# Kernel tuning notes

Measured on AMD Instinct MI355X. Metric: run time of the kernel, lower is better.

The kernel has to match this reference:

```python
import jax, jax.numpy as jnp
import numpy as np

EMBED = 1024
HEADS = 16
HEAD_DIM = EMBED // HEADS


def setup_inputs() -> dict:
    key = jax.random.key(0)
    k1, k2, k3, k4, k5 = jax.random.split(key, 5)
    B, S = 4, 2048
    scale = 1.0 / np.sqrt(EMBED)
    return {
        "query_features": jax.random.normal(k1, (B, S, EMBED), dtype=jnp.float32),
        "W_qkv": jax.random.normal(k2, (EMBED, 3 * EMBED), dtype=jnp.float32) * scale,
        "b_qkv": jnp.zeros((3 * EMBED,), dtype=jnp.float32),
        "W_out": jax.random.normal(k3, (EMBED, EMBED), dtype=jnp.float32) * scale,
        "b_out": jnp.zeros((EMBED,), dtype=jnp.float32),
    }


def reference(query_features, W_qkv, b_qkv, W_out, b_out):
    B, S, E = query_features.shape
    qkv = jnp.einsum("bse,ef->bsf", query_features, W_qkv) + b_qkv  # [B,S,3E]
    q, k, v = jnp.split(qkv, 3, axis=-1)
    # split heads: [B,H,S,D]
    def heads(x):
        return x.reshape(B, S, HEADS, HEAD_DIM).transpose(0, 2, 1, 3)
    q, k, v = heads(q), heads(k), heads(v)
    scale = 1.0 / np.sqrt(HEAD_DIM)
    scores = jnp.einsum("bhqd,bhkd->bhqk", q, k) * scale
    attn = jax.nn.softmax(scores, axis=-1)
    out = jnp.einsum("bhqk,bhkd->bhqd", attn, v)  # [B,H,S,D]
    out = out.transpose(0, 2, 1, 3).reshape(B, S, E)
    return jnp.einsum("bse,ef->bsf", out, W_out) + b_out
```

## Files before the change

kernel.cpp:

```cpp
#include <hip/hip_runtime.h>
#include <hip/hip_bf16.h>
#include <stdint.h>
#include <stddef.h>

using short8  = __attribute__((ext_vector_type(8))) short;
using short4v = __attribute__((ext_vector_type(4))) short;
using int4v   = __attribute__((ext_vector_type(4))) int;
using f32x4   = __attribute__((ext_vector_type(4))) float;
typedef __hip_bfloat16 bf16_t;

__device__ __forceinline__ void glds16(const void* g, const void* l) {
  __builtin_amdgcn_global_load_lds(
      (const __attribute__((address_space(1))) void*)g,
      (__attribute__((address_space(3))) void*)l, 16, 0, 0);
}
__device__ __forceinline__ short bfbits(float x) {
  bf16_t h = __float2bfloat16(x);
  return __builtin_bit_cast(short, h);
}
__device__ __forceinline__ int pk2(float lo, float hi) {
  return __builtin_amdgcn_perm(__builtin_bit_cast(unsigned, hi),
                               __builtin_bit_cast(unsigned, lo), 0x07060302u);
}

__global__ __launch_bounds__(256)
void preprocess(const void* __restrict__ Wqkv, bf16_t* __restrict__ WqkvT,
                const void* __restrict__ Wout, bf16_t* __restrict__ WoutT,
                const void* __restrict__ Xv, bf16_t* __restrict__ Xb,
                int* __restrict__ flag) {
  __shared__ int sbad;
  __shared__ float tile[32][33];
  const int tid = threadIdx.x;
  const int bid = blockIdx.x;
  if (tid == 0) sbad = 0;
  __syncthreads();
  {
    int bad = 0;
    const unsigned short* wp = (const unsigned short*)Wqkv;
#pragma unroll
    for (int j = 0; j < 4; ++j) {
      float f = __uint_as_float((unsigned)wp[tid + j * 256] << 16);
      if (!(fabsf(f) <= 1e10f)) bad = 1;
    }
    if (bad) sbad = 1;
  }
  __syncthreads();
  const int isf = sbad;
  if (bid == 0 && tid == 0) *flag = isf;

  if (bid < 4096) {
    int bx = bid & 127;
    const int by = bid >> 7;
    const int tx = tid & 31, ty = tid >> 5;
    const void* Wv;
    bf16_t* Wt;
    int C;
    if (bx < 96) {
      Wv = Wqkv; Wt = WqkvT; C = 3072;
    } else {
      bx -= 96; Wv = Wout; Wt = WoutT; C = 1024;
    }
    const int n0 = bx * 32, k0 = by * 32;
#pragma unroll
    for (int j = 0; j < 4; ++j) {
      const int k = k0 + ty + j * 8;
      tile[ty + j * 8][tx] =
          isf ? ((const float*)Wv)[(size_t)k * C + n0 + tx]
              : __bfloat162float(((const bf16_t*)Wv)[(size_t)k * C + n0 + tx]);
    }
    __syncthreads();
#pragma unroll
    for (int j = 0; j < 4; ++j) {
      const int n = n0 + ty + j * 8;
      Wt[(size_t)n * 1024 + k0 + tx] = __float2bfloat16(tile[tx][ty + j * 8]);
    }
  } else {
    const int i = ((bid - 4096) * 256 + tid) * 4;
    if (isf) {
      const float4 v = *(const float4*)((const float*)Xv + i);
      Xb[i + 0] = __float2bfloat16(v.x);
      Xb[i + 1] = __float2bfloat16(v.y);
      Xb[i + 2] = __float2bfloat16(v.z);
      Xb[i + 3] = __float2bfloat16(v.w);
    } else {
      *(uint2*)(Xb + i) = *(const uint2*)((const bf16_t*)Xv + i);
    }
  }
}

template <int MODE>
__global__ __launch_bounds__(256)
void gemm_k(const bf16_t* __restrict__ A, const bf16_t* __restrict__ Bt,
            const void* __restrict__ biasv, void* __restrict__ Cv,
            bf16_t* __restrict__ Qo, bf16_t* __restrict__ Ko,
            bf16_t* __restrict__ Vo, int M, int N, int K,
            const int* __restrict__ flag) {
  constexpr float CSC = 0.18033688011112042f;
  __shared__ __align__(16) bf16_t lA[128 * 64];
  __shared__ __align__(16) bf16_t lB[128 * 64];

  const int isf32 = *flag;
  const int tid  = threadIdx.x;
  const int w    = tid >> 6;
  const int lane = tid & 63;
  const int lrow = lane & 15;
  const int quad = lane >> 4;
  const int m0 = blockIdx.x * 128;
  const int n0 = blockIdx.y * 128;
  const int wm = (w >> 1) * 64;
  const int wn = (w & 1) * 64;

  f32x4 acc[4][4];
  for (int i = 0; i < 4; ++i)
    for (int j = 0; j < 4; ++j)
      for (int r = 0; r < 4; ++r) acc[i][j][r] = 0.f;

  for (int kt = 0; kt < K; kt += 64) {
#pragma unroll
    for (int i = 0; i < 4; ++i) {
      const int cbase = i * 256 + w * 64;
      const int c = cbase + lane;
      const int row = c >> 3;
      const int q = (c & 7) ^ (row & 7);
      glds16(A + (size_t)(m0 + row) * K + kt + q * 8,
             (const char*)lA + cbase * 16);
      glds16(Bt + (size_t)(n0 + row) * K + kt + q * 8,
             (const char*)lB + cbase * 16);
    }
    __syncthreads();
#pragma unroll
    for (int ks = 0; ks < 2; ++ks) {
      short8 af[4], bfr[4];
#pragma unroll
      for (int mi = 0; mi < 4; ++mi) {
        const int row = wm + mi * 16 + lrow;
        const int slot = (ks * 4 + quad) ^ (row & 7);
        af[mi] = *(const short8*)((const char*)lA + row * 128 + slot * 16);
      }
#pragma unroll
      for (int ni = 0; ni < 4; ++ni) {
        const int row = wn + ni * 16 + lrow;
        const int slot = (ks * 4 + quad) ^ (row & 7);
        bfr[ni] = *(const short8*)((const char*)lB + row * 128 + slot * 16);
      }
#pragma unroll
      for (int mi = 0; mi < 4; ++mi)
#pragma unroll
        for (int ni = 0; ni < 4; ++ni)
          acc[mi][ni] = __builtin_amdgcn_mfma_f32_16x16x32_bf16(
              af[mi], bfr[ni], acc[mi][ni], 0, 0, 0);
    }
    __syncthreads();
  }

  if (MODE == 1) {
    const int sec = n0 >> 10;
    const int b = m0 >> 11;
    const int s0 = (m0 & 2047) + wm + quad * 4;
#pragma unroll
    for (int mi = 0; mi < 4; ++mi) {
#pragma unroll
      for (int ni = 0; ni < 4; ++ni) {
        const int col = n0 + wn + ni * 16 + lrow;
        const float bv = isf32 ? ((const float*)biasv)[col]
                               : __bfloat162float(((const bf16_t*)biasv)[col]);
        const int h = (col >> 6) & 15, d = col & 63;
        const int s = s0 + mi * 16;
        if (sec == 2) {
          short4v hv4;
#pragma unroll
          for (int r = 0; r < 4; ++r) hv4[r] = bfbits(acc[mi][ni][r] + bv);
          *(short4v*)(Vo + ((((size_t)b * 16 + h) * 64) + d) * 2048 + s) = hv4;
        } else if (sec == 0) {
          bf16_t* dst = Qo + ((((size_t)b * 16 + h) * 2048) + s) * 64 + d;
#pragma unroll
          for (int r = 0; r < 4; ++r)
            dst[(size_t)r * 64] = __float2bfloat16((acc[mi][ni][r] + bv) * CSC);
        } else {
          bf16_t* dst = Ko + ((((size_t)b * 16 + h) * 2048) + s) * 64 + d;
#pragma unroll
          for (int r = 0; r < 4; ++r)
            dst[(size_t)r * 64] = __float2bfloat16(acc[mi][ni][r] + bv);
        }
      }
    }
  } else {
#pragma unroll
    for (int mi = 0; mi < 4; ++mi) {
#pragma unroll
      for (int ni = 0; ni < 4; ++ni) {
        const int col = n0 + wn + ni * 16 + lrow;
        const float bv = isf32 ? ((const float*)biasv)[col]
                               : __bfloat162float(((const bf16_t*)biasv)[col]);
#pragma unroll
        for (int r = 0; r < 4; ++r) {
          const int row = m0 + wm + mi * 16 + quad * 4 + r;
          const float val = acc[mi][ni][r] + bv;
          if (isf32)
            ((float*)Cv)[(size_t)row * N + col] = val;
          else
            ((bf16_t*)Cv)[(size_t)row * N + col] = __float2bfloat16(val);
        }
      }
    }
  }
}

__global__ __launch_bounds__(256, 2)
void attn_fwd(const bf16_t* __restrict__ Q, const bf16_t* __restrict__ K,
              const bf16_t* __restrict__ Vt, bf16_t* __restrict__ AO) {
  __shared__ __align__(16) bf16_t lK[2][64 * 64];
  __shared__ __align__(16) bf16_t lV[2][64 * 64];

  const int tid  = threadIdx.x;
  const int w    = tid >> 6;
  const int lane = tid & 63;
  const int lrow = lane & 15;
  const int quad = lane >> 4;
  const int id = blockIdx.x;
  const int swz = (id & 7) * 64 + (id >> 3);
  const int bh  = swz >> 3;
  const int q0  = (swz & 7) * 256;

  const bf16_t* Qb = Q + (size_t)bh * 2048 * 64;
  const bf16_t* Kb = K + (size_t)bh * 2048 * 64;
  const bf16_t* Vb = Vt + (size_t)bh * 64 * 2048;

  const int rbase = (lrow >> 2) * 8 + (lrow & 3);
  const int fkl   = 2 * (lrow >> 2) + (lrow & 1);

  short8 aq[4][2];
#pragma unroll
  for (int qt = 0; qt < 4; ++qt)
#pragma unroll
    for (int ks = 0; ks < 2; ++ks)
      aq[qt][ks] = *(const short8*)(Qb +
          (size_t)(q0 + w * 64 + qt * 16 + lrow) * 64 + ks * 32 + quad * 8);

  short8 ones;
#pragma unroll
  for (int j = 0; j < 8; ++j) ones[j] = (short)0x3F80;

  const f32x4 zf = {0.f, 0.f, 0.f, 0.f};

  f32x4 ot[4][4];
  f32x4 lsacc[4];
#pragma unroll
  for (int dt = 0; dt < 4; ++dt)
#pragma unroll
    for (int qt = 0; qt < 4; ++qt)
#pragma unroll
      for (int r = 0; r < 4; ++r) ot[dt][qt][r] = 0.f;
#pragma unroll
  for (int qt = 0; qt < 4; ++qt)
#pragma unroll
    for (int r = 0; r < 4; ++r) lsacc[qt][r] = 0.f;

  auto stage = [&](int buf, int kt) {
#pragma unroll
    for (int i = 0; i < 2; ++i) {
      const int cbase = i * 256 + w * 64;
      const int c = cbase + lane;
      const int row = c >> 3, ch = c & 7;
      const int fk = 2 * ((row >> 3) & 3) + (row & 1);
      glds16(Kb + (size_t)(kt + row) * 64 + (ch ^ fk) * 8,
             (const char*)lK[buf] + cbase * 16);
      glds16(Vb + (size_t)row * 2048 + kt + (ch ^ (row & 7)) * 8,
             (const char*)lV[buf] + cbase * 16);
    }
  };

  auto compute = [&](const bf16_t* lKb, const bf16_t* lVb) {
#pragma unroll
    for (int g = 0; g < 2; ++g) {
      short8 ak0[2], ak1[2];
#pragma unroll
      for (int T = 0; T < 2; ++T) {
        const int row = g * 32 + T * 4 + rbase;
        ak0[T] = *(const short8*)((const char*)lKb + row * 128 +
                                  ((0 * 4 + quad) ^ fkl) * 16);
        ak1[T] = *(const short8*)((const char*)lKb + row * 128 +
                                  ((1 * 4 + quad) ^ fkl) * 16);
      }
      f32x4 sc[2][4];
      __builtin_amdgcn_s_setprio(1);
#pragma unroll
      for (int T = 0; T < 2; ++T)
#pragma unroll
        for (int qt = 0; qt < 4; ++qt)
          sc[T][qt] = __builtin_amdgcn_mfma_f32_16x16x32_bf16(
              ak0[T], aq[qt][0], zf, 0, 0, 0);
#pragma unroll
      for (int T = 0; T < 2; ++T)
#pragma unroll
        for (int qt = 0; qt < 4; ++qt)
          sc[T][qt] = __builtin_amdgcn_mfma_f32_16x16x32_bf16(
              ak1[T], aq[qt][1], sc[T][qt], 0, 0, 0);
      __builtin_amdgcn_s_setprio(0);

      short8 pb[4];
#pragma unroll
      for (int qt = 0; qt < 4; ++qt) {
        float p[8];
#pragma unroll
        for (int T = 0; T < 2; ++T)
#pragma unroll
          for (int r = 0; r < 4; ++r)
            p[T * 4 + r] = __builtin_amdgcn_exp2f(sc[T][qt][r]);
        int4v pi = {pk2(p[0], p[1]), pk2(p[2], p[3]), pk2(p[4], p[5]),
                    pk2(p[6], p[7])};
        pb[qt] = __builtin_bit_cast(short8, pi);
      }

      __builtin_amdgcn_s_setprio(1);
#pragma unroll
      for (int qt = 0; qt < 4; ++qt)
        lsacc[qt] = __builtin_amdgcn_mfma_f32_16x16x32_bf16(ones, pb[qt],
                                                            lsacc[qt], 0, 0, 0);
#pragma unroll
      for (int dt = 0; dt < 4; ++dt) {
        const int row = dt * 16 + lrow;
        const int slot = (g * 4 + quad) ^ (row & 7);
        const short8 vf =
            *(const short8*)((const char*)lVb + row * 128 + slot * 16);
#pragma unroll
        for (int qt = 0; qt < 4; ++qt)
          ot[dt][qt] = __builtin_amdgcn_mfma_f32_16x16x32_bf16(
              vf, pb[qt], ot[dt][qt], 0, 0, 0);
      }
      __builtin_amdgcn_s_setprio(0);
    }
  };

  stage(0, 0);
  __syncthreads();

  for (int kt = 0; kt < 2048; kt += 128) {
    if (kt + 64 < 2048) stage(1, kt + 64);
    compute(lK[0], lV[0]);
    __syncthreads();
    if (kt + 128 < 2048) stage(0, kt + 128);
    compute(lK[1], lV[1]);
    __syncthreads();
  }

  const int b = bh >> 4, h = bh & 15;
#pragma unroll
  for (int qt = 0; qt < 4; ++qt) {
    const float inv = 1.f / lsacc[qt][0];
    const int srow = q0 + w * 64 + qt * 16 + lrow;
#pragma unroll
    for (int dt = 0; dt < 4; ++dt) {
      uint2 pack;
      short* ps = (short*)&pack;
#pragma unroll
      for (int r = 0; r < 4; ++r) ps[r] = bfbits(ot[dt][qt][r] * inv);
      *(uint2*)(AO + ((size_t)b * 2048 + srow) * 1024 + h * 64 + dt * 16 +
                quad * 4) = pack;
    }
  }
}

extern "C" void kernel_launch(void* const* d_in, const int* in_sizes, int n_in,
                              void* d_out, int out_size, void* d_ws,
                              size_t ws_size, hipStream_t stream) {
  const void* X    = d_in[0];
  const void* Wqkv = d_in[1];
  const void* bqkv = d_in[2];
  const void* Wout = d_in[3];
  const void* bout = d_in[4];

  char* ws = (char*)d_ws;
  bf16_t* WqkvT = (bf16_t*)(ws);
  bf16_t* WoutT = (bf16_t*)(ws + 6291456);
  bf16_t* Qw    = (bf16_t*)(ws + 8388608);
  bf16_t* Kw    = (bf16_t*)(ws + 25165824);
  bf16_t* Vw    = (bf16_t*)(ws + 41943040);
  bf16_t* AOw   = (bf16_t*)(ws + 58720256);
  bf16_t* Xbf   = AOw;
  int*    flag  = (int*)(ws + 75497472);

  preprocess<<<12288, 256, 0, stream>>>(Wqkv, WqkvT, Wout, WoutT, X, Xbf, flag);

  gemm_k<1><<<dim3(64, 24), 256, 0, stream>>>(Xbf, WqkvT, bqkv, nullptr, Qw,
                                              Kw, Vw, 8192, 3072, 1024, flag);
  attn_fwd<<<512, 256, 0, stream>>>(Qw, Kw, Vw, AOw);
  gemm_k<0><<<dim3(64, 8), 256, 0, stream>>>(AOw, WoutT, bout, d_out, nullptr,
                                             nullptr, nullptr, 8192, 1024, 1024,
                                             flag);
}
```

Measured before the change: 257.1 us.

## Double-buffer GEMM LDS tiles and precompute staging address offsets

The GEMM kernel gets double-buffered LDS tiles, so the next K-tile's global-to-LDS loads are issued before computing on the current tile, and one barrier per iteration is removed. Per-thread global and LDS offsets are precomputed once for both the GEMM and attention staging, cutting address arithmetic in the loop. The attention loop is rewritten as a single loop over chunks with parity buffer selection. This doubles GEMM LDS use to 64KB, which can lower occupancy, and uses 32-bit offsets that assume small tensors.

```diff
diff --git a/kernel.cpp b/kernel.cpp
--- a/kernel.cpp
+++ b/kernel.cpp
@@ -96,8 +96,8 @@
             bf16_t* __restrict__ Vo, int M, int N, int K,
             const int* __restrict__ flag) {
   constexpr float CSC = 0.18033688011112042f;
-  __shared__ __align__(16) bf16_t lA[128 * 64];
-  __shared__ __align__(16) bf16_t lB[128 * 64];
+  __shared__ __align__(16) bf16_t lA[2][128 * 64];
+  __shared__ __align__(16) bf16_t lB[2][128 * 64];
 
   const int isf32 = *flag;
   const int tid  = threadIdx.x;
@@ -115,19 +115,38 @@
     for (int j = 0; j < 4; ++j)
       for (int r = 0; r < 4; ++r) acc[i][j][r] = 0.f;
 
+  const char* Ab = (const char*)A;
+  const char* Bb = (const char*)Bt;
+  unsigned aoff[4], boff[4];
+  int ldst[4];
+#pragma unroll
+  for (int i = 0; i < 4; ++i) {
+    const int cbase = i * 256 + w * 64;
+    const int c = cbase + lane;
+    const int row = c >> 3;
+    const int q = (c & 7) ^ (row & 7);
+    aoff[i] = (unsigned)((m0 + row) * K + q * 8) * 2u;
+    boff[i] = (unsigned)((n0 + row) * K + q * 8) * 2u;
+    ldst[i] = cbase * 16;
+  }
+
+  auto stage = [&](int buf, int kt) {
+    const unsigned kb = (unsigned)kt * 2u;
+#pragma unroll
+    for (int i = 0; i < 4; ++i) {
+      glds16(Ab + aoff[i] + kb, (const char*)lA[buf] + ldst[i]);
+      glds16(Bb + boff[i] + kb, (const char*)lB[buf] + ldst[i]);
+    }
+  };
+
+  stage(0, 0);
+  __syncthreads();
+
+  int buf = 0;
   for (int kt = 0; kt < K; kt += 64) {
-#pragma unroll
-    for (int i = 0; i < 4; ++i) {
-      const int cbase = i * 256 + w * 64;
-      const int c = cbase + lane;
-      const int row = c >> 3;
-      const int q = (c & 7) ^ (row & 7);
-      glds16(A + (size_t)(m0 + row) * K + kt + q * 8,
-             (const char*)lA + cbase * 16);
-      glds16(Bt + (size_t)(n0 + row) * K + kt + q * 8,
-             (const char*)lB + cbase * 16);
-    }
-    __syncthreads();
+    if (kt + 64 < K) stage(buf ^ 1, kt + 64);
+    const char* la = (const char*)lA[buf];
+    const char* lb = (const char*)lB[buf];
 #pragma unroll
     for (int ks = 0; ks < 2; ++ks) {
       short8 af[4], bfr[4];
@@ -135,13 +154,13 @@
       for (int mi = 0; mi < 4; ++mi) {
         const int row = wm + mi * 16 + lrow;
         const int slot = (ks * 4 + quad) ^ (row & 7);
-        af[mi] = *(const short8*)((const char*)lA + row * 128 + slot * 16);
+        af[mi] = *(const short8*)(la + row * 128 + slot * 16);
       }
 #pragma unroll
       for (int ni = 0; ni < 4; ++ni) {
         const int row = wn + ni * 16 + lrow;
         const int slot = (ks * 4 + quad) ^ (row & 7);
-        bfr[ni] = *(const short8*)((const char*)lB + row * 128 + slot * 16);
+        bfr[ni] = *(const short8*)(lb + row * 128 + slot * 16);
       }
 #pragma unroll
       for (int mi = 0; mi < 4; ++mi)
@@ -151,6 +170,7 @@
               af[mi], bfr[ni], acc[mi][ni], 0, 0, 0);
     }
     __syncthreads();
+    buf ^= 1;
   }
 
   if (MODE == 1) {
@@ -223,8 +243,8 @@
   const int q0  = (swz & 7) * 256;
 
   const bf16_t* Qb = Q + (size_t)bh * 2048 * 64;
-  const bf16_t* Kb = K + (size_t)bh * 2048 * 64;
-  const bf16_t* Vb = Vt + (size_t)bh * 64 * 2048;
+  const char* Kbc = (const char*)(K + (size_t)bh * 2048 * 64);
+  const char* Vbc = (const char*)(Vt + (size_t)bh * 64 * 2048);
 
   const int rbase = (lrow >> 2) * 8 + (lrow & 3);
   const int fkl   = 2 * (lrow >> 2) + (lrow & 1);
@@ -256,17 +276,26 @@
 #pragma unroll
     for (int r = 0; r < 4; ++r) lsacc[qt][r] = 0.f;
 
-  auto stage = [&](int buf, int kt) {
+  unsigned kgo[2], vgo[2];
+  int ldst[2];
+#pragma unroll
+  for (int i = 0; i < 2; ++i) {
+    const int cbase = i * 256 + w * 64;
+    const int c = cbase + lane;
+    const int row = c >> 3, ch = c & 7;
+    const int fk = 2 * ((row >> 3) & 3) + (row & 1);
+    kgo[i] = (unsigned)(row * 128 + (ch ^ fk) * 16);
+    vgo[i] = (unsigned)(row * 4096 + (ch ^ (row & 7)) * 16);
+    ldst[i] = cbase * 16;
+  }
+
+  auto stage = [&](int buf, int cidx) {
+    const unsigned kb = (unsigned)cidx * 8192u;
+    const unsigned vb = (unsigned)cidx * 128u;
 #pragma unroll
     for (int i = 0; i < 2; ++i) {
-      const int cbase = i * 256 + w * 64;
-      const int c = cbase + lane;
-      const int row = c >> 3, ch = c & 7;
-      const int fk = 2 * ((row >> 3) & 3) + (row & 1);
-      glds16(Kb + (size_t)(kt + row) * 64 + (ch ^ fk) * 8,
-             (const char*)lK[buf] + cbase * 16);
-      glds16(Vb + (size_t)row * 2048 + kt + (ch ^ (row & 7)) * 8,
-             (const char*)lV[buf] + cbase * 16);
+      glds16(Kbc + kgo[i] + kb, (const char*)lK[buf] + ldst[i]);
+      glds16(Vbc + vgo[i] + vb, (const char*)lV[buf] + ldst[i]);
     }
   };
 
@@ -335,12 +364,9 @@
   stage(0, 0);
   __syncthreads();
 
-  for (int kt = 0; kt < 2048; kt += 128) {
-    if (kt + 64 < 2048) stage(1, kt + 64);
-    compute(lK[0], lV[0]);
-    __syncthreads();
-    if (kt + 128 < 2048) stage(0, kt + 128);
-    compute(lK[1], lV[1]);
+  for (int c = 0; c < 32; ++c) {
+    if (c + 1 < 32) stage((c + 1) & 1, c + 1);
+    compute(lK[c & 1], lV[c & 1]);
     __syncthreads();
   }
 
```

Result: no change. 255.8 us (-0.5%).
